# Kernel tuning notes

Measured on AMD Instinct MI355X. Metric: run time of the kernel, lower is better.

## Reference

```python
import jax, jax.numpy as jnp
import numpy as np

EPS = 1e-5

def _proj(x, W, g, b, m, v):
    # 1x1 conv (no bias) + BatchNorm2d (inference stats) + ReLU
    y = jnp.einsum('bchw,oc->bohw', x, W)
    scale = g / jnp.sqrt(v + EPS)
    y = y * scale[:, None, None] + (b - m * scale)[:, None, None]
    return jax.nn.relu(y)

def setup_inputs() -> dict:
    key = jax.random.key(0)
    B, C, H, W = 4, 192, 64, 64
    ks = jax.random.split(key, 10)
    d = {
        'lr_hsi': jax.random.normal(ks[0], (B, C, H, W), jnp.float32),
        'refine_hsi': jax.random.normal(ks[1], (B, C, H, W), jnp.float32),
    }
    for i, name in enumerate(['q', 'k', 'v', 't']):
        d['W' + name] = jax.random.normal(ks[2 + i], (C, C), jnp.float32) * 0.05
        d['g' + name] = jnp.ones((C,), jnp.float32)
        d['b' + name] = jnp.zeros((C,), jnp.float32)
        d['m' + name] = jnp.zeros((C,), jnp.float32)
        d['v' + name] = jnp.ones((C,), jnp.float32)
    return d

def reference(lr_hsi, refine_hsi,
              Wq, gq, bq, mq, vq,
              Wk, gk, bk, mk, vk,
              Wv, gv, bv, mv, vv,
              Wt, gt, bt, mt, vt):
    B, C, H, W = refine_hsi.shape
    HW = H * W
    q = _proj(refine_hsi, Wq, gq, bq, mq, vq).reshape(B, C, HW).transpose(0, 2, 1)  # [B, HWq, C]
    k = _proj(lr_hsi, Wk, gk, bk, mk, vk).reshape(B, C, HW)                          # [B, C, HWk]
    v = _proj(lr_hsi, Wv, gv, bv, mv, vv).reshape(B, C, HW).transpose(0, 2, 1)      # [B, HWk, C]
    corr = jnp.einsum('bqc,bck->bqk', q, k) * (C ** -0.5)  # [B, HWq, HWk]
    corr = jax.nn.softmax(corr, axis=1)  # NOTE: softmax over the QUERY axis (dim=1), as in source
    ss = jnp.einsum('bqk,bkc->bqc', corr, v)               # [B, HWq, C]
    ss = ss.transpose(0, 2, 1).reshape(B, C, H, W)
    out = _proj(ss, Wt, gt, bt, mt, vt)
    return (out, corr)
```

## Files before the change

kernel.cpp:

```cpp
#include <hip/hip_runtime.h>
#include <math.h>

typedef __attribute__((ext_vector_type(4))) float f32x4;
typedef __attribute__((ext_vector_type(8))) short bf16x8;

__device__ __forceinline__ unsigned short f2bf(float f) {
  unsigned int u = __builtin_bit_cast(unsigned int, f);
  u += 0x7FFFu + ((u >> 16) & 1u);
  return (unsigned short)(u >> 16);
}

__device__ __forceinline__ float bf2f(unsigned short u) {
  return __builtin_bit_cast(float, (unsigned int)u << 16);
}

__device__ __forceinline__ f32x4 mfma16(bf16x8 a, bf16x8 b, f32x4 c) {
  return __builtin_amdgcn_mfma_f32_16x16x32_bf16(a, b, c, 0, 0, 0);
}

__global__ void prep_kernel(const float* __restrict__ W, const float* __restrict__ g,
                            const float* __restrict__ bb, const float* __restrict__ mm,
                            const float* __restrict__ vv,
                            unsigned short* __restrict__ Wout, float* __restrict__ bout,
                            float alpha) {
  int idx = blockIdx.x * 256 + threadIdx.x;
  if (idx < 192 * 192) {
    int o = idx / 192;
    float s = g[o] * rsqrtf(vv[o] + 1e-5f);
    Wout[idx] = f2bf(W[idx] * s * alpha);
  }
  if (idx < 192) {
    float s = g[idx] * rsqrtf(vv[idx] + 1e-5f);
    bout[idx] = (bb[idx] - mm[idx] * s) * alpha;
  }
}

template <int LAYOUT>
__launch_bounds__(256)
__global__ void proj_kernel(const float* __restrict__ X,
                            const unsigned short* __restrict__ Wp,
                            const float* __restrict__ bias,
                            unsigned short* __restrict__ Yv) {
  const int o0 = blockIdx.x * 64;
  const int hw0 = blockIdx.y * 64;
  const int b = blockIdx.z;
  const int w = threadIdx.x >> 6, l = threadIdx.x & 63;
  const int l16 = l & 15, lg = l >> 4;
  const float* Xb = X + (size_t)b * 192 * 4096;

  f32x4 acc[4] = {f32x4{0,0,0,0}, f32x4{0,0,0,0}, f32x4{0,0,0,0}, f32x4{0,0,0,0}};

  for (int ks = 0; ks < 6; ++ks) {
    const int c0 = ks * 32 + lg * 8;
    bf16x8 a = *(const bf16x8*)(Wp + (size_t)(o0 + 16 * w + l16) * 192 + c0);
#pragma unroll
    for (int n = 0; n < 4; ++n) {
      const int hw = hw0 + 16 * n + l16;
      bf16x8 bfr;
#pragma unroll
      for (int j = 0; j < 8; ++j)
        bfr[j] = (short)f2bf(Xb[(size_t)(c0 + j) * 4096 + hw]);
      acc[n] = mfma16(a, bfr, acc[n]);
    }
  }

#pragma unroll
  for (int n = 0; n < 4; ++n) {
    const int hw = hw0 + 16 * n + l16;
    float vv4[4];
#pragma unroll
    for (int r = 0; r < 4; ++r) {
      const int o = o0 + 16 * w + lg * 4 + r;
      vv4[r] = fmaxf(acc[n][r] + bias[o], 0.0f);
    }
    if (LAYOUT == 1) {
      unsigned int lo = (unsigned)f2bf(vv4[0]) | ((unsigned)f2bf(vv4[1]) << 16);
      unsigned int hi = (unsigned)f2bf(vv4[2]) | ((unsigned)f2bf(vv4[3]) << 16);
      uint2 pk; pk.x = lo; pk.y = hi;
      *(uint2*)(Yv + ((size_t)b * 4096 + hw) * 192 + o0 + 16 * w + lg * 4) = pk;
    } else {
#pragma unroll
      for (int r = 0; r < 4; ++r) {
        const int o = o0 + 16 * w + lg * 4 + r;
        Yv[((size_t)b * 192 + o) * 4096 + hw] = f2bf(vv4[r]);
      }
    }
  }
}

template <int NS>
__launch_bounds__(256)
__global__ void proj_sum_kernel(const float* __restrict__ X,
                                const unsigned short* __restrict__ Wp,
                                const float* __restrict__ bias,
                                float* __restrict__ Yv) {
  const int o0 = blockIdx.x * 64;
  const int hw0 = blockIdx.y * 64;
  const int b = blockIdx.z;
  const int w = threadIdx.x >> 6, l = threadIdx.x & 63;
  const int l16 = l & 15, lg = l >> 4;
  const float* Xb = X + (size_t)b * 192 * 4096;
  const size_t sstride = (size_t)4 * 192 * 4096;

  f32x4 acc[4] = {f32x4{0,0,0,0}, f32x4{0,0,0,0}, f32x4{0,0,0,0}, f32x4{0,0,0,0}};

  for (int ks = 0; ks < 6; ++ks) {
    const int c0 = ks * 32 + lg * 8;
    bf16x8 a = *(const bf16x8*)(Wp + (size_t)(o0 + 16 * w + l16) * 192 + c0);
#pragma unroll
    for (int n = 0; n < 4; ++n) {
      const int hw = hw0 + 16 * n + l16;
      bf16x8 bfr;
#pragma unroll
      for (int j = 0; j < 8; ++j) {
        float s = Xb[(size_t)(c0 + j) * 4096 + hw];
#pragma unroll
        for (int ss = 1; ss < NS; ++ss)
          s += Xb[(size_t)(c0 + j) * 4096 + hw + ss * sstride];
        bfr[j] = (short)f2bf(s);
      }
      acc[n] = mfma16(a, bfr, acc[n]);
    }
  }

#pragma unroll
  for (int n = 0; n < 4; ++n) {
    const int hw = hw0 + 16 * n + l16;
#pragma unroll
    for (int r = 0; r < 4; ++r) {
      const int o = o0 + 16 * w + lg * 4 + r;
      Yv[((size_t)b * 192 + o) * 4096 + hw] = fmaxf(acc[n][r] + bias[o], 0.0f);
    }
  }
}

__launch_bounds__(256)
__global__ void pass1_e_kernel(const unsigned short* __restrict__ qp,
                               const unsigned short* __restrict__ kpT,
                               unsigned short* __restrict__ E,
                               float* __restrict__ colsum) {
  const int q0 = blockIdx.x * 128, k0 = blockIdx.y * 128, b = blockIdx.z;
  const int w = threadIdx.x >> 6, l = threadIdx.x & 63;
  const int l16 = l & 15, lg = l >> 4;
  const unsigned short* qb = qp + (size_t)b * 4096 * 192;
  const unsigned short* kb = kpT + (size_t)b * 4096 * 192;

  __shared__ __align__(16) unsigned short smem[128 * 200];

  {
    const int t = threadIdx.x;
#pragma unroll
    for (int i = 0; i < 12; ++i) {
      int idx = t + i * 256;
      int row = idx / 24, cu = idx % 24;
      uint4 vdat = *(const uint4*)(qb + (size_t)(q0 + row) * 192 + cu * 8);
      *(uint4*)&smem[row * 200 + cu * 8] = vdat;
    }
  }
  __syncthreads();

  f32x4 acc[2][8];
#pragma unroll
  for (int m = 0; m < 2; ++m)
#pragma unroll
    for (int n = 0; n < 8; ++n) acc[m][n] = f32x4{0, 0, 0, 0};

  for (int ks = 0; ks < 6; ++ks) {
    const int c0 = ks * 32 + lg * 8;
    bf16x8 a0 = *(const bf16x8*)(kb + (size_t)(k0 + 32 * w + l16) * 192 + c0);
    bf16x8 a1 = *(const bf16x8*)(kb + (size_t)(k0 + 32 * w + 16 + l16) * 192 + c0);
#pragma unroll
    for (int n = 0; n < 8; ++n) {
      bf16x8 bfr = *(const bf16x8*)&smem[(16 * n + l16) * 200 + c0];
      acc[0][n] = mfma16(a0, bfr, acc[0][n]);
      acc[1][n] = mfma16(a1, bfr, acc[1][n]);
    }
  }

#pragma unroll
  for (int m = 0; m < 2; ++m) {
#pragma unroll
    for (int r = 0; r < 4; ++r) {
      float s = 0.f;
#pragma unroll
      for (int n = 0; n < 8; ++n) {
        float e = __builtin_amdgcn_exp2f(acc[m][n][r]);
        acc[m][n][r] = e;
        s += e;
      }
      s += __shfl_xor(s, 1);
      s += __shfl_xor(s, 2);
      s += __shfl_xor(s, 4);
      s += __shfl_xor(s, 8);
      if (l16 == 0)
        atomicAdd(&colsum[(size_t)b * 4096 + k0 + 32 * w + 16 * m + lg * 4 + r], s);
    }
  }

  __syncthreads();
#pragma unroll
  for (int m = 0; m < 2; ++m)
#pragma unroll
    for (int n = 0; n < 8; ++n) {
      unsigned int lo = (unsigned)f2bf(acc[m][n][0]) | ((unsigned)f2bf(acc[m][n][1]) << 16);
      unsigned int hi = (unsigned)f2bf(acc[m][n][2]) | ((unsigned)f2bf(acc[m][n][3]) << 16);
      uint2 pk; pk.x = lo; pk.y = hi;
      *(uint2*)&smem[(16 * n + l16) * 144 + 32 * w + 16 * m + lg * 4] = pk;
    }
  __syncthreads();

  {
    const int t = threadIdx.x;
#pragma unroll
    for (int i = 0; i < 8; ++i) {
      int idx = t + i * 256;
      int row = idx >> 4, c16 = idx & 15;
      uint4 vdat = *(const uint4*)&smem[row * 144 + c16 * 8];
      *(uint4*)(E + (size_t)(b * 4096 + q0 + row) * 4096 + k0 + c16 * 8) = vdat;
    }
  }
}

__global__ void invert_kernel(float* __restrict__ p, int n) {
  int i = blockIdx.x * 256 + threadIdx.x;
  if (i < n) p[i] = 1.0f / p[i];
}

__launch_bounds__(256)
__global__ void vscale_kernel(const unsigned short* __restrict__ vp,
                              const float* __restrict__ rcol,
                              unsigned short* __restrict__ vps) {
  int i = blockIdx.x * 256 + threadIdx.x;
  if (i >= 4 * 192 * 512) return;
  int b = i / (192 * 512);
  int k = (i & 511) * 8;
  f32x4 rc0 = *(const f32x4*)(rcol + b * 4096 + k);
  f32x4 rc1 = *(const f32x4*)(rcol + b * 4096 + k + 4);
  bf16x8 v = *(const bf16x8*)(vp + (size_t)i * 8);
  bf16x8 o;
#pragma unroll
  for (int j = 0; j < 4; ++j) {
    o[j] = (short)f2bf(bf2f((unsigned short)v[j]) * rc0[j]);
    o[j + 4] = (short)f2bf(bf2f((unsigned short)v[j + 4]) * rc1[j]);
  }
  *(bf16x8*)(vps + (size_t)i * 8) = o;
}

__launch_bounds__(512)
__global__ void pv_kernel(const unsigned short* __restrict__ E,
                          const unsigned short* __restrict__ vps,
                          float* __restrict__ ssP) {
  const int q0 = blockIdx.x * 128;
  const int s = blockIdx.y;
  const int b = blockIdx.z;
  const int w = threadIdx.x >> 6, l = threadIdx.x & 63;
  const int l16 = l & 15, lg = l >> 4;
  const unsigned short* Eb = E + (size_t)b * 4096 * 4096;
  const unsigned short* vb = vps + (size_t)b * 192 * 4096;
  float* ssb = ssP + (size_t)(s * 4 + b) * 192 * 4096;

  __shared__ __align__(16) unsigned short Est[128][72];
  __shared__ __align__(16) unsigned short Vst[192][72];

  f32x4 ssa[12];
#pragma unroll
  for (int j = 0; j < 12; ++j) ssa[j] = f32x4{0, 0, 0, 0};

  const int kc0 = s * 16;
  for (int kc = kc0; kc < kc0 + 16; ++kc) {
    const int k0 = kc * 64;
    {
      const int t = threadIdx.x;
#pragma unroll
      for (int i = 0; i < 2; ++i) {
        int idx = t + i * 512;
        int row = idx >> 3, c8 = idx & 7;
        uint4 vdat = *(const uint4*)(Eb + (size_t)(q0 + row) * 4096 + k0 + c8 * 8);
        *(uint4*)&Est[row][c8 * 8] = vdat;
      }
#pragma unroll
      for (int i = 0; i < 3; ++i) {
        int idx = t + i * 512;
        int row = idx >> 3, c8 = idx & 7;
        uint4 vdat = *(const uint4*)(vb + (size_t)row * 4096 + k0 + c8 * 8);
        *(uint4*)&Vst[row][c8 * 8] = vdat;
      }
    }
    __syncthreads();
#pragma unroll
    for (int kstep = 0; kstep < 2; ++kstep) {
      bf16x8 af = *(const bf16x8*)&Est[16 * w + l16][kstep * 32 + lg * 8];
#pragma unroll
      for (int j = 0; j < 12; ++j) {
        bf16x8 bfr = *(const bf16x8*)&Vst[16 * j + l16][kstep * 32 + lg * 8];
        ssa[j] = mfma16(af, bfr, ssa[j]);
      }
    }
    __syncthreads();
  }

#pragma unroll
  for (int j = 0; j < 12; ++j)
    *(f32x4*)(ssb + (size_t)(16 * j + l16) * 4096 + q0 + 16 * w + lg * 4) = ssa[j];
}

__launch_bounds__(256)
__global__ void corr_kernel(const unsigned short* __restrict__ E,
                            const float* __restrict__ rcol,
                            float* __restrict__ corr) {
  const size_t N = (size_t)4 * 4096 * 512;
  for (size_t i = (size_t)blockIdx.x * 256 + threadIdx.x; i < N; i += (size_t)gridDim.x * 256) {
    size_t bq = i >> 9;
    int k = ((int)i & 511) * 8;
    int b = (int)(bq >> 12);
    bf16x8 e = *(const bf16x8*)(E + bq * 4096 + k);
    f32x4 rc0 = *(const f32x4*)(rcol + b * 4096 + k);
    f32x4 rc1 = *(const f32x4*)(rcol + b * 4096 + k + 4);
    f32x4 o0, o1;
#pragma unroll
    for (int j = 0; j < 4; ++j) {
      o0[j] = bf2f((unsigned short)e[j]) * rc0[j];
      o1[j] = bf2f((unsigned short)e[j + 4]) * rc1[j];
    }
    __builtin_nontemporal_store(o0, (f32x4*)(corr + bq * 4096 + k));
    __builtin_nontemporal_store(o1, (f32x4*)(corr + bq * 4096 + k + 4));
  }
}

__launch_bounds__(256)
__global__ void pass1_basic_kernel(const unsigned short* __restrict__ qp,
                                   const unsigned short* __restrict__ kpT,
                                   float* __restrict__ colsum) {
  const int q0 = blockIdx.x * 128, k0 = blockIdx.y * 128, b = blockIdx.z;
  const int w = threadIdx.x >> 6, l = threadIdx.x & 63;
  const int l16 = l & 15, lg = l >> 4;
  const unsigned short* qb = qp + (size_t)b * 4096 * 192;
  const unsigned short* kb = kpT + (size_t)b * 4096 * 192;

  __shared__ __align__(16) unsigned short kpl[128][200];
  __shared__ float cs[4][128];

  {
    const int t = threadIdx.x;
#pragma unroll
    for (int i = 0; i < 12; ++i) {
      int idx = t + i * 256;
      int row = idx / 24, cu = idx % 24;
      uint4 vdat = *(const uint4*)(kb + (size_t)(k0 + row) * 192 + cu * 8);
      *(uint4*)&kpl[row][cu * 8] = vdat;
    }
  }
  __syncthreads();

  f32x4 acc[2][8];
#pragma unroll
  for (int m = 0; m < 2; ++m)
#pragma unroll
    for (int n = 0; n < 8; ++n) acc[m][n] = f32x4{0, 0, 0, 0};

  for (int ks = 0; ks < 6; ++ks) {
    const int c0 = ks * 32 + lg * 8;
    bf16x8 a0 = *(const bf16x8*)(qb + (size_t)(q0 + 32 * w + l16) * 192 + c0);
    bf16x8 a1 = *(const bf16x8*)(qb + (size_t)(q0 + 32 * w + 16 + l16) * 192 + c0);
#pragma unroll
    for (int n = 0; n < 8; ++n) {
      bf16x8 bfr = *(const bf16x8*)&kpl[16 * n + l16][c0];
      acc[0][n] = mfma16(a0, bfr, acc[0][n]);
      acc[1][n] = mfma16(a1, bfr, acc[1][n]);
    }
  }

  float part[8];
#pragma unroll
  for (int n = 0; n < 8; ++n) {
    float s = 0.f;
#pragma unroll
    for (int r = 0; r < 4; ++r)
      s += __builtin_amdgcn_exp2f(acc[0][n][r]) + __builtin_amdgcn_exp2f(acc[1][n][r]);
    s += __shfl_xor(s, 16);
    s += __shfl_xor(s, 32);
    part[n] = s;
  }
  if (l < 16) {
#pragma unroll
    for (int n = 0; n < 8; ++n) cs[w][16 * n + l] = part[n];
  }
  __syncthreads();
  const int t = threadIdx.x;
  if (t < 128) {
    float s = cs[0][t] + cs[1][t] + cs[2][t] + cs[3][t];
    atomicAdd(&colsum[(size_t)b * 4096 + k0 + t], s);
  }
}

template <int NS>
__launch_bounds__(512)
__global__ void pass2_basic_kernel(const unsigned short* __restrict__ qp,
                                   const unsigned short* __restrict__ kpT,
                                   const unsigned short* __restrict__ vpN,
                                   const float* __restrict__ rcol,
                                   float* __restrict__ corr,
                                   float* __restrict__ ssP) {
  const int q0 = blockIdx.x * 64;
  const int s = blockIdx.y;
  const int b = blockIdx.z;
  const int kc0 = s * (32 / NS);
  const int w = threadIdx.x >> 6, l = threadIdx.x & 63;
  const int l16 = l & 15, lg = l >> 4;
  const int mw = w & 1, nw = w >> 1;
  const unsigned short* qb = qp + (size_t)b * 4096 * 192;
  const unsigned short* kb = kpT + (size_t)b * 4096 * 192;
  const unsigned short* vb = vpN + (size_t)b * 192 * 4096;
  const float* rc = rcol + (size_t)b * 4096;
  float* corb = corr + (size_t)b * 4096 * 4096;
  float* ssb = ssP + (size_t)(s * 4 + b) * 192 * 4096;

  __shared__ __align__(16) float cor[64][132];

  bf16x8 af[2][6];
#pragma unroll
  for (int tm = 0; tm < 2; ++tm)
#pragma unroll
    for (int ks = 0; ks < 6; ++ks)
      af[tm][ks] = *(const bf16x8*)(qb + (size_t)(q0 + 16 * (2 * mw + tm) + l16) * 192 + ks * 32 + lg * 8);

  f32x4 ssa[2][3];
#pragma unroll
  for (int tm = 0; tm < 2; ++tm)
#pragma unroll
    for (int j = 0; j < 3; ++j) ssa[tm][j] = f32x4{0, 0, 0, 0};

  for (int kc = kc0; kc < kc0 + 32 / NS; ++kc) {
    const int k0 = kc * 128;
    f32x4 sa[2][2];
#pragma unroll
    for (int tm = 0; tm < 2; ++tm)
#pragma unroll
      for (int tn = 0; tn < 2; ++tn) sa[tm][tn] = f32x4{0, 0, 0, 0};

    for (int ks = 0; ks < 6; ++ks) {
      const int c0 = ks * 32 + lg * 8;
#pragma unroll
      for (int tn = 0; tn < 2; ++tn) {
        const int kcol = k0 + 16 * (2 * nw + tn) + l16;
        bf16x8 bfr = *(const bf16x8*)(kb + (size_t)kcol * 192 + c0);
        sa[0][tn] = mfma16(af[0][ks], bfr, sa[0][tn]);
        sa[1][tn] = mfma16(af[1][ks], bfr, sa[1][tn]);
      }
    }
    float rcv[2];
#pragma unroll
    for (int tn = 0; tn < 2; ++tn) rcv[tn] = rc[k0 + 16 * (2 * nw + tn) + l16];
#pragma unroll
    for (int tm = 0; tm < 2; ++tm)
#pragma unroll
      for (int tn = 0; tn < 2; ++tn)
#pragma unroll
        for (int r = 0; r < 4; ++r)
          sa[tm][tn][r] = __builtin_amdgcn_exp2f(sa[tm][tn][r]) * rcv[tn];

    __syncthreads();
#pragma unroll
    for (int tm = 0; tm < 2; ++tm)
#pragma unroll
      for (int tn = 0; tn < 2; ++tn) {
        const int col = 16 * (2 * nw + tn) + l16;
#pragma unroll
        for (int r = 0; r < 4; ++r)
          cor[16 * (2 * mw + tm) + lg * 4 + r][col] = sa[tm][tn][r];
      }
    __syncthreads();

    {
      const int t = threadIdx.x;
#pragma unroll
      for (int it = 0; it < 4; ++it) {
        int idx = t + it * 512;
        int row = idx >> 5, seg = idx & 31;
        f32x4 v4 = *(const f32x4*)&cor[row][seg * 4];
        __builtin_nontemporal_store(v4, (f32x4*)(corb + (size_t)(q0 + row) * 4096 + k0 + seg * 4));
      }
    }

#pragma unroll
    for (int ks2 = 0; ks2 < 4; ++ks2) {
      const int cc = ks2 * 32 + lg * 8;
      bf16x8 pa[2];
#pragma unroll
      for (int tm = 0; tm < 2; ++tm) {
        f32x4 p0 = *(const f32x4*)&cor[16 * (2 * mw + tm) + l16][cc];
        f32x4 p1 = *(const f32x4*)&cor[16 * (2 * mw + tm) + l16][cc + 4];
#pragma unroll
        for (int j = 0; j < 4; ++j) {
          pa[tm][j] = (short)f2bf(p0[j]);
          pa[tm][j + 4] = (short)f2bf(p1[j]);
        }
      }
#pragma unroll
      for (int j = 0; j < 3; ++j) {
        const int ccol = 16 * (nw + 4 * j) + l16;
        bf16x8 bfr = *(const bf16x8*)(vb + (size_t)ccol * 4096 + k0 + cc);
        ssa[0][j] = mfma16(pa[0], bfr, ssa[0][j]);
        ssa[1][j] = mfma16(pa[1], bfr, ssa[1][j]);
      }
    }
  }

#pragma unroll
  for (int tm = 0; tm < 2; ++tm)
#pragma unroll
    for (int j = 0; j < 3; ++j) {
      const int ccol = 16 * (nw + 4 * j) + l16;
#pragma unroll
      for (int r = 0; r < 4; ++r) {
        const int qrow = q0 + 16 * (2 * mw + tm) + lg * 4 + r;
        ssb[(size_t)ccol * 4096 + qrow] = ssa[tm][j][r];
      }
    }
}

extern "C" void kernel_launch(void* const* d_in, const int* in_sizes, int n_in,
                              void* d_out, int out_size, void* d_ws, size_t ws_size,
                              hipStream_t stream) {
  (void)in_sizes; (void)n_in; (void)out_size;
  const float* lr = (const float*)d_in[0];
  const float* refine = (const float*)d_in[1];

  char* ws = (char*)d_ws;
  unsigned short* w4 = (unsigned short*)(ws + 0);
  float* bias4 = (float*)(ws + 294912);
  unsigned short* qp = (unsigned short*)(ws + 297984);
  unsigned short* kp = (unsigned short*)(ws + 297984 + 6291456);
  unsigned short* vp = (unsigned short*)(ws + 297984 + 2 * 6291456);
  float* colsum = (float*)(ws + 19172352);
  unsigned short* vps = (unsigned short*)(ws + 19237888);
  float* ssP = (float*)(ws + 25529344);
  unsigned short* Ebuf = (unsigned short*)(ws + 75860992);
  const size_t NEW_NEED = 210078720;

  float* out0 = (float*)d_out;
  float* corr = out0 + 3145728;

  const float alpha = (float)(1.4426950408889634 / sqrt(192.0));

  for (int p = 0; p < 4; ++p) {
    prep_kernel<<<dim3(144), dim3(256), 0, stream>>>(
        (const float*)d_in[2 + 5 * p], (const float*)d_in[3 + 5 * p],
        (const float*)d_in[4 + 5 * p], (const float*)d_in[5 + 5 * p],
        (const float*)d_in[6 + 5 * p],
        w4 + p * 36864, bias4 + p * 192, p == 0 ? alpha : 1.0f);
  }
  hipMemsetAsync(colsum, 0, 65536, stream);

  proj_kernel<1><<<dim3(3, 64, 4), dim3(256), 0, stream>>>(refine, w4, bias4, qp);
  proj_kernel<1><<<dim3(3, 64, 4), dim3(256), 0, stream>>>(lr, w4 + 36864, bias4 + 192, kp);
  proj_kernel<0><<<dim3(3, 64, 4), dim3(256), 0, stream>>>(lr, w4 + 2 * 36864, bias4 + 2 * 192, vp);

  if (ws_size >= NEW_NEED) {
    pass1_e_kernel<<<dim3(32, 32, 4), dim3(256), 0, stream>>>(qp, kp, Ebuf, colsum);
    invert_kernel<<<dim3(64), dim3(256), 0, stream>>>(colsum, 16384);
    vscale_kernel<<<dim3(1536), dim3(256), 0, stream>>>(vp, colsum, vps);
    pv_kernel<<<dim3(32, 4, 4), dim3(512), 0, stream>>>(Ebuf, vps, ssP);
    proj_sum_kernel<4><<<dim3(3, 64, 4), dim3(256), 0, stream>>>(ssP, w4 + 3 * 36864, bias4 + 3 * 192, out0);
    corr_kernel<<<dim3(2048), dim3(256), 0, stream>>>(Ebuf, colsum, corr);
  } else {
    pass1_basic_kernel<<<dim3(32, 32, 4), dim3(256), 0, stream>>>(qp, kp, colsum);
    invert_kernel<<<dim3(64), dim3(256), 0, stream>>>(colsum, 16384);
    pass2_basic_kernel<2><<<dim3(64, 2, 4), dim3(512), 0, stream>>>(qp, kp, vp, colsum, corr, ssP);
    proj_sum_kernel<2><<<dim3(3, 64, 4), dim3(256), 0, stream>>>(ssP, w4 + 3 * 36864, bias4 + 3 * 192, out0);
  }
}
```

Before: 293.5 us.

## Prefetch next E/V tile into registers and retile PV warps as 2x6

The PV kernel now loads the next k-chunk of E and V from global memory into registers while the current chunk is being multiplied, so global load latency overlaps with MFMA work. Each wave is also remapped from one 16-row q strip across all 12 channel fragments to two q fragments by six channel fragments. This cuts the shared-memory fragment reads per MFMA. The cost is extra register pressure from the staged uint4 values.

```diff
diff --git a/kernel.cpp b/kernel.cpp
--- a/kernel.cpp
+++ b/kernel.cpp
@@ -255,6 +255,7 @@
   const int b = blockIdx.z;
   const int w = threadIdx.x >> 6, l = threadIdx.x & 63;
   const int l16 = l & 15, lg = l >> 4;
+  const int qg = w >> 1, cg = w & 1;
   const unsigned short* Eb = E + (size_t)b * 4096 * 4096;
   const unsigned short* vb = vps + (size_t)b * 192 * 4096;
   float* ssb = ssP + (size_t)(s * 4 + b) * 192 * 4096;
@@ -262,46 +263,67 @@
   __shared__ __align__(16) unsigned short Est[128][72];
   __shared__ __align__(16) unsigned short Vst[192][72];
 
-  f32x4 ssa[12];
-#pragma unroll
-  for (int j = 0; j < 12; ++j) ssa[j] = f32x4{0, 0, 0, 0};
+  const int t = threadIdx.x;
+  const int erow = t >> 3, ec8 = t & 7;
+
+  f32x4 ssa[2][6];
+#pragma unroll
+  for (int qf = 0; qf < 2; ++qf)
+#pragma unroll
+    for (int j = 0; j < 6; ++j) ssa[qf][j] = f32x4{0, 0, 0, 0};
 
   const int kc0 = s * 16;
+
+  uint4 se[2], sv[3];
+  {
+    const int k0 = kc0 * 64;
+#pragma unroll
+    for (int i = 0; i < 2; ++i)
+      se[i] = *(const uint4*)(Eb + (size_t)(q0 + erow + i * 64) * 4096 + k0 + ec8 * 8);
+#pragma unroll
+    for (int i = 0; i < 3; ++i)
+      sv[i] = *(const uint4*)(vb + (size_t)(erow + i * 64) * 4096 + k0 + ec8 * 8);
+  }
+
   for (int kc = kc0; kc < kc0 + 16; ++kc) {
-    const int k0 = kc * 64;
-    {
-      const int t = threadIdx.x;
-#pragma unroll
-      for (int i = 0; i < 2; ++i) {
-        int idx = t + i * 512;
-        int row = idx >> 3, c8 = idx & 7;
-        uint4 vdat = *(const uint4*)(Eb + (size_t)(q0 + row) * 4096 + k0 + c8 * 8);
-        *(uint4*)&Est[row][c8 * 8] = vdat;
-      }
-#pragma unroll
-      for (int i = 0; i < 3; ++i) {
-        int idx = t + i * 512;
-        int row = idx >> 3, c8 = idx & 7;
-        uint4 vdat = *(const uint4*)(vb + (size_t)row * 4096 + k0 + c8 * 8);
-        *(uint4*)&Vst[row][c8 * 8] = vdat;
-      }
-    }
+#pragma unroll
+    for (int i = 0; i < 2; ++i) *(uint4*)&Est[erow + i * 64][ec8 * 8] = se[i];
+#pragma unroll
+    for (int i = 0; i < 3; ++i) *(uint4*)&Vst[erow + i * 64][ec8 * 8] = sv[i];
     __syncthreads();
+
+    if (kc + 1 < kc0 + 16) {
+      const int k0n = (kc + 1) * 64;
+#pragma unroll
+      for (int i = 0; i < 2; ++i)
+        se[i] = *(const uint4*)(Eb + (size_t)(q0 + erow + i * 64) * 4096 + k0n + ec8 * 8);
+#pragma unroll
+      for (int i = 0; i < 3; ++i)
+        sv[i] = *(const uint4*)(vb + (size_t)(erow + i * 64) * 4096 + k0n + ec8 * 8);
+    }
+
 #pragma unroll
     for (int kstep = 0; kstep < 2; ++kstep) {
-      bf16x8 af = *(const bf16x8*)&Est[16 * w + l16][kstep * 32 + lg * 8];
-#pragma unroll
-      for (int j = 0; j < 12; ++j) {
-        bf16x8 bfr = *(const bf16x8*)&Vst[16 * j + l16][kstep * 32 + lg * 8];
-        ssa[j] = mfma16(af, bfr, ssa[j]);
+      const int koff = kstep * 32 + lg * 8;
+      bf16x8 af0 = *(const bf16x8*)&Est[qg * 32 + l16][koff];
+      bf16x8 af1 = *(const bf16x8*)&Est[qg * 32 + 16 + l16][koff];
+#pragma unroll
+      for (int j = 0; j < 6; ++j) {
+        bf16x8 bfr = *(const bf16x8*)&Vst[cg * 96 + 16 * j + l16][koff];
+        ssa[0][j] = mfma16(af0, bfr, ssa[0][j]);
+        ssa[1][j] = mfma16(af1, bfr, ssa[1][j]);
       }
     }
     __syncthreads();
   }
 
 #pragma unroll
-  for (int j = 0; j < 12; ++j)
-    *(f32x4*)(ssb + (size_t)(16 * j + l16) * 4096 + q0 + 16 * w + lg * 4) = ssa[j];
+  for (int qf = 0; qf < 2; ++qf)
+#pragma unroll
+    for (int j = 0; j < 6; ++j) {
+      const int c = cg * 96 + 16 * j + l16;
+      *(f32x4*)(ssb + (size_t)c * 4096 + q0 + qg * 32 + qf * 16 + lg * 4) = ssa[qf][j];
+    }
 }
 
 __launch_bounds__(256)
```

Result: slower. 339.4 us (+15.6%).
